# Performance work log

Measured on AMD Instinct MI355X. Metric: run time of the kernel, lower is better.

## Reference

```python
import jax, jax.numpy as jnp
import numpy as np

DIM = 768
NUM_HEADS = 12
HIDDEN = int(DIM * 4.0)
EPS = 1e-5


def setup_inputs() -> dict:
    key = jax.random.key(0)
    ks = jax.random.split(key, 8)
    s = lambda k, shape, scale=0.02: jax.random.normal(k, shape, dtype=jnp.float32) * scale
    return {
        "x": jax.random.normal(ks[0], (8, 1024, DIM), dtype=jnp.float32),
        "ln1_g": jnp.ones((DIM,), jnp.float32),
        "ln1_b": jnp.zeros((DIM,), jnp.float32),
        "qkv_w": s(ks[1], (DIM, 3 * DIM)),
        "qkv_b": jnp.zeros((3 * DIM,), jnp.float32),
        "proj_w": s(ks[2], (DIM, DIM)),
        "proj_b": jnp.zeros((DIM,), jnp.float32),
        "ln2_g": jnp.ones((DIM,), jnp.float32),
        "ln2_b": jnp.zeros((DIM,), jnp.float32),
        "fc1_w": s(ks[3], (DIM, HIDDEN)),
        "fc1_b": jnp.zeros((HIDDEN,), jnp.float32),
        "fc2_w": s(ks[4], (HIDDEN, DIM)),
        "fc2_b": jnp.zeros((DIM,), jnp.float32),
    }


def layer_norm(x, g, b):
    mu = jnp.mean(x, axis=-1, keepdims=True)
    var = jnp.mean(jnp.square(x - mu), axis=-1, keepdims=True)
    return (x - mu) * jax.lax.rsqrt(var + EPS) * g + b


def reference(x, ln1_g, ln1_b, qkv_w, qkv_b, proj_w, proj_b,
              ln2_g, ln2_b, fc1_w, fc1_b, fc2_w, fc2_b):
    B, N, C = x.shape
    H = NUM_HEADS
    Dh = C // H
    scale = Dh ** -0.5

    # --- Attention (pre-norm) ---
    h = layer_norm(x, ln1_g, ln1_b)
    qkv = h @ qkv_w + qkv_b                       # [B, N, 3C]
    qkv = qkv.reshape(B, N, 3, H, Dh)
    q, k, v = qkv[:, :, 0], qkv[:, :, 1], qkv[:, :, 2]  # [B, N, H, Dh]
    attn = jnp.einsum("bqhd,bkhd->bhqk", q, k) * scale  # [B, H, N, N]
    attn = jax.nn.softmax(attn, axis=-1)
    o = jnp.einsum("bhqk,bkhd->bqhd", attn, v).reshape(B, N, C)
    x = x + (o @ proj_w + proj_b)

    # --- MLP (pre-norm) ---
    h = layer_norm(x, ln2_g, ln2_b)
    h = jax.nn.gelu(h @ fc1_w + fc1_b, approximate=False)  # torch nn.GELU = exact erf
    x = x + (h @ fc2_w + fc2_b)
    return x
```

## Files before the change

kernel.cpp:

```cpp
#include <hip/hip_runtime.h>
#include <hip/hip_bf16.h>
#include <cstdint>

using f32x4  = __attribute__((ext_vector_type(4))) float;
using bf16x8 = __attribute__((ext_vector_type(8))) short;

__device__ inline ushort f2bf(float f) {
    union { float f; uint u; } x; x.f = f;
    uint u = x.u;
    return (ushort)((u + 0x7FFFu + ((u >> 16) & 1u)) >> 16);
}

__device__ inline void unpack8(uint4 v, float* out) {
    uint ws[4] = {v.x, v.y, v.z, v.w};
#pragma unroll
    for (int i = 0; i < 4; ++i) {
        union { uint u; float f; } lo, hi;
        lo.u = ws[i] << 16;
        hi.u = ws[i] & 0xFFFF0000u;
        out[2 * i]     = lo.f;
        out[2 * i + 1] = hi.f;
    }
}

__device__ inline void gload16(const ushort* g, ushort* lds) {
    __builtin_amdgcn_global_load_lds(
        (const __attribute__((address_space(1))) unsigned int*)g,
        (__attribute__((address_space(3))) unsigned int*)lds, 16, 0, 0);
}

__global__ __launch_bounds__(256) void transpose_cast(const float* __restrict__ w,
                                                      ushort* __restrict__ wt,
                                                      int K, int N) {
    __shared__ float tile[32][33];
    const int bn = blockIdx.x * 32;
    const int bk = blockIdx.y * 32;
    const int tx = threadIdx.x & 31, ty = threadIdx.x >> 5;
#pragma unroll
    for (int i = 0; i < 32; i += 8)
        tile[ty + i][tx] = w[(size_t)(bk + ty + i) * N + bn + tx];
    __syncthreads();
#pragma unroll
    for (int i = 0; i < 32; i += 8)
        wt[(size_t)(bn + ty + i) * K + bk + tx] = f2bf(tile[tx][ty + i]);
}

__global__ __launch_bounds__(256) void ln_bf16(const float* __restrict__ x,
                                               const float* __restrict__ g,
                                               const float* __restrict__ b,
                                               ushort* __restrict__ out) {
    const int row = blockIdx.x;
    const float* xr = x + (size_t)row * 768;
    const int t = threadIdx.x;
    float v0 = xr[t], v1 = xr[t + 256], v2 = xr[t + 512];
    float s  = v0 + v1 + v2;
    float sq = v0 * v0 + v1 * v1 + v2 * v2;
#pragma unroll
    for (int off = 32; off > 0; off >>= 1) {
        s  += __shfl_down(s, off);
        sq += __shfl_down(sq, off);
    }
    __shared__ float sa[4], sb[4];
    const int wv = t >> 6, lane = t & 63;
    if (lane == 0) { sa[wv] = s; sb[wv] = sq; }
    __syncthreads();
    s  = sa[0] + sa[1] + sa[2] + sa[3];
    sq = sb[0] + sb[1] + sb[2] + sb[3];
    const float mu   = s * (1.0f / 768.0f);
    const float var  = sq * (1.0f / 768.0f) - mu * mu;
    const float rstd = rsqrtf(var + 1e-5f);
    ushort* orow = out + (size_t)row * 768;
    orow[t]       = f2bf((v0 - mu) * rstd * g[t]       + b[t]);
    orow[t + 256] = f2bf((v1 - mu) * rstd * g[t + 256] + b[t + 256]);
    orow[t + 512] = f2bf((v2 - mu) * rstd * g[t + 512] + b[t + 512]);
}

template <int EPI>
__global__ __launch_bounds__(256) void gemm_bt(const ushort* __restrict__ A,
                                               const ushort* __restrict__ Bt,
                                               const float* __restrict__ bias,
                                               const float* __restrict__ resid,
                                               void* __restrict__ out,
                                               int M, int N, int K) {
    __shared__ ushort As[128 * 32];
    __shared__ ushort Bs[128 * 32];
    const int t    = threadIdx.x;
    const int lane = t & 63;
    const int w    = t >> 6;
    const int wr   = w >> 1, wc = w & 1;
    const int bm   = blockIdx.y * 128, bn = blockIdx.x * 128;
    const int lr   = lane >> 4, lc = lane & 15;
    const int srow = lane >> 2;
    const int sk8  = (lane & 3) * 8;

    const f32x4 fzero = {0.f, 0.f, 0.f, 0.f};
    f32x4 acc[4][4];
#pragma unroll
    for (int ai = 0; ai < 4; ++ai)
#pragma unroll
        for (int bj = 0; bj < 4; ++bj) acc[ai][bj] = fzero;

    const ushort* Ag0 = A  + (size_t)(bm + w * 16 + srow) * K + sk8;
    const ushort* Ag1 = Ag0 + (size_t)64 * K;
    const ushort* Bg0 = Bt + (size_t)(bn + w * 16 + srow) * K + sk8;
    const ushort* Bg1 = Bg0 + (size_t)64 * K;
    ushort* lA0 = &As[(w * 16) * 32];
    ushort* lA1 = &As[(64 + w * 16) * 32];
    ushort* lB0 = &Bs[(w * 16) * 32];
    ushort* lB1 = &Bs[(64 + w * 16) * 32];

    for (int kb = 0; kb < K; kb += 32) {
        __syncthreads();
        gload16(Ag0 + kb, lA0);
        gload16(Ag1 + kb, lA1);
        gload16(Bg0 + kb, lB0);
        gload16(Bg1 + kb, lB1);
        __syncthreads();
        bf16x8 af[4], bf[4];
#pragma unroll
        for (int ai = 0; ai < 4; ++ai)
            af[ai] = *(const bf16x8*)&As[(wr * 64 + ai * 16 + lc) * 32 + lr * 8];
#pragma unroll
        for (int bj = 0; bj < 4; ++bj)
            bf[bj] = *(const bf16x8*)&Bs[(wc * 64 + bj * 16 + lc) * 32 + lr * 8];
#pragma unroll
        for (int ai = 0; ai < 4; ++ai)
#pragma unroll
            for (int bj = 0; bj < 4; ++bj)
                acc[ai][bj] = __builtin_amdgcn_mfma_f32_16x16x32_bf16(af[ai], bf[bj],
                                                                      acc[ai][bj], 0, 0, 0);
    }

#pragma unroll
    for (int ai = 0; ai < 4; ++ai) {
#pragma unroll
        for (int bj = 0; bj < 4; ++bj) {
            int col  = bn + wc * 64 + bj * 16 + lc;
            float bs = bias[col];
#pragma unroll
            for (int j = 0; j < 4; ++j) {
                int row   = bm + wr * 64 + ai * 16 + lr * 4 + j;
                float val = acc[ai][bj][j] + bs;
                if (EPI == 1) {
                    val += resid[(size_t)row * N + col];
                    ((float*)out)[(size_t)row * N + col] = val;
                } else if (EPI == 2) {
                    val = 0.5f * val * (1.0f + erff(val * 0.70710678118f));
                    ((ushort*)out)[(size_t)row * N + col] = f2bf(val);
                } else {
                    ((ushort*)out)[(size_t)row * N + col] = f2bf(val);
                }
            }
        }
    }
}

__global__ __launch_bounds__(256) void attn_mfma(const ushort* __restrict__ qkv,
                                                 ushort* __restrict__ outb) {
    __shared__ ushort Kls[64 * 72];
    __shared__ ushort Vtls[64 * 72];
    __shared__ ushort Pls[4][32 * 72];

    const int bid = blockIdx.x;
    const int b   = bid / 96;
    const int rem = bid % 96;
    const int h   = rem >> 3;
    const int qc  = rem & 7;
    const int t    = threadIdx.x;
    const int w    = t >> 6;
    const int lane = t & 63;
    const int lr   = lane >> 4, lc = lane & 15;
    const int q0   = qc * 128 + w * 32;
    const size_t bbase = (size_t)b * 1024;

    bf16x8 qa[2][2];
#pragma unroll
    for (int rt = 0; rt < 2; ++rt)
#pragma unroll
        for (int ds = 0; ds < 2; ++ds) {
            uint4 u = *(const uint4*)(qkv + (bbase + q0 + rt * 16 + lc) * 2304 +
                                      h * 64 + ds * 32 + lr * 8);
            float tmp[8];
            unpack8(u, tmp);
            bf16x8 v;
#pragma unroll
            for (int j = 0; j < 8; ++j) v[j] = (short)f2bf(tmp[j] * 0.125f);
            qa[rt][ds] = v;
        }

    const f32x4 fzero = {0.f, 0.f, 0.f, 0.f};
    f32x4 O[2][4];
    float m[2][4], l[2][4];
#pragma unroll
    for (int rt = 0; rt < 2; ++rt) {
#pragma unroll
        for (int dt = 0; dt < 4; ++dt) O[rt][dt] = fzero;
#pragma unroll
        for (int j = 0; j < 4; ++j) { m[rt][j] = -INFINITY; l[rt][j] = 0.0f; }
    }

    for (int kt = 0; kt < 16; ++kt) {
        const int k0 = kt * 64;
        __syncthreads();
#pragma unroll
        for (int i = 0; i < 2; ++i) {
            int idx = t + i * 256;
            int key = idx >> 3, seg = idx & 7;
            uint4 u = *(const uint4*)(qkv + (bbase + k0 + key) * 2304 + 768 +
                                      h * 64 + seg * 8);
            *(uint4*)&Kls[key * 72 + seg * 8] = u;
        }
        {
            int key = t & 63, dblk = t >> 6;
#pragma unroll
            for (int i = 0; i < 2; ++i) {
                int d0 = dblk * 8 + i * 32;
                uint4 u = *(const uint4*)(qkv + (bbase + k0 + key) * 2304 + 1536 +
                                          h * 64 + d0);
                const ushort* us = (const ushort*)&u;
#pragma unroll
                for (int j = 0; j < 8; ++j) Vtls[(d0 + j) * 72 + key] = us[j];
            }
        }
        __syncthreads();

        f32x4 s4[2][4];
#pragma unroll
        for (int rt = 0; rt < 2; ++rt)
#pragma unroll
            for (int kt4 = 0; kt4 < 4; ++kt4) {
                f32x4 acc = fzero;
#pragma unroll
                for (int ds = 0; ds < 2; ++ds) {
                    bf16x8 kb = *(const bf16x8*)&Kls[(kt4 * 16 + lc) * 72 + ds * 32 + lr * 8];
                    acc = __builtin_amdgcn_mfma_f32_16x16x32_bf16(qa[rt][ds], kb, acc, 0, 0, 0);
                }
                s4[rt][kt4] = acc;
            }

#pragma unroll
        for (int rt = 0; rt < 2; ++rt) {
#pragma unroll
            for (int j = 0; j < 4; ++j) {
                float v = fmaxf(fmaxf(s4[rt][0][j], s4[rt][1][j]),
                                fmaxf(s4[rt][2][j], s4[rt][3][j]));
#pragma unroll
                for (int off = 1; off < 16; off <<= 1) v = fmaxf(v, __shfl_xor(v, off));
                float mn = fmaxf(m[rt][j], v);
                float c  = __expf(m[rt][j] - mn);
                m[rt][j] = mn;
                float psum = 0.f;
#pragma unroll
                for (int kt4 = 0; kt4 < 4; ++kt4) {
                    float p = __expf(s4[rt][kt4][j] - mn);
                    s4[rt][kt4][j] = p;
                    psum += p;
                }
#pragma unroll
                for (int off = 1; off < 16; off <<= 1) psum += __shfl_xor(psum, off);
                l[rt][j] = l[rt][j] * c + psum;
#pragma unroll
                for (int dt = 0; dt < 4; ++dt) O[rt][dt][j] *= c;
                int prow = rt * 16 + lr * 4 + j;
#pragma unroll
                for (int kt4 = 0; kt4 < 4; ++kt4)
                    Pls[w][prow * 72 + kt4 * 16 + lc] = f2bf(s4[rt][kt4][j]);
            }
        }

        bf16x8 pa[2][2];
#pragma unroll
        for (int rt = 0; rt < 2; ++rt)
#pragma unroll
            for (int ks = 0; ks < 2; ++ks)
                pa[rt][ks] = *(const bf16x8*)&Pls[w][(rt * 16 + lc) * 72 + ks * 32 + lr * 8];
#pragma unroll
        for (int dt = 0; dt < 4; ++dt)
#pragma unroll
            for (int ks = 0; ks < 2; ++ks) {
                bf16x8 vb = *(const bf16x8*)&Vtls[(dt * 16 + lc) * 72 + ks * 32 + lr * 8];
#pragma unroll
                for (int rt = 0; rt < 2; ++rt)
                    O[rt][dt] = __builtin_amdgcn_mfma_f32_16x16x32_bf16(pa[rt][ks], vb,
                                                                        O[rt][dt], 0, 0, 0);
            }
    }

#pragma unroll
    for (int rt = 0; rt < 2; ++rt)
#pragma unroll
        for (int j = 0; j < 4; ++j) {
            float inv = 1.0f / l[rt][j];
            size_t row = bbase + q0 + rt * 16 + lr * 4 + j;
#pragma unroll
            for (int dt = 0; dt < 4; ++dt)
                outb[row * 768 + h * 64 + dt * 16 + lc] = f2bf(O[rt][dt][j] * inv);
        }
}

extern "C" void kernel_launch(void* const* d_in, const int* in_sizes, int n_in,
                              void* d_out, int out_size, void* d_ws, size_t ws_size,
                              hipStream_t stream) {
    const float* x      = (const float*)d_in[0];
    const float* ln1_g  = (const float*)d_in[1];
    const float* ln1_b  = (const float*)d_in[2];
    const float* qkv_w  = (const float*)d_in[3];
    const float* qkv_b  = (const float*)d_in[4];
    const float* proj_w = (const float*)d_in[5];
    const float* proj_b = (const float*)d_in[6];
    const float* ln2_g  = (const float*)d_in[7];
    const float* ln2_b  = (const float*)d_in[8];
    const float* fc1_w  = (const float*)d_in[9];
    const float* fc1_b  = (const float*)d_in[10];
    const float* fc2_w  = (const float*)d_in[11];
    const float* fc2_b  = (const float*)d_in[12];

    char* ws = (char*)d_ws;
    auto alloc = [&](size_t bytes) {
        char* p = ws;
        ws += (bytes + 255) & ~(size_t)255;
        return p;
    };
    ushort* qkv_wt  = (ushort*)alloc((size_t)768 * 2304 * 2);
    ushort* proj_wt = (ushort*)alloc((size_t)768 * 768 * 2);
    ushort* fc1_wt  = (ushort*)alloc((size_t)768 * 3072 * 2);
    ushort* fc2_wt  = (ushort*)alloc((size_t)3072 * 768 * 2);
    ushort* hb      = (ushort*)alloc((size_t)8192 * 768 * 2);
    ushort* qkvb    = (ushort*)alloc((size_t)8192 * 2304 * 2);
    ushort* ob      = (ushort*)alloc((size_t)8192 * 768 * 2);
    float*  x1      = (float*)alloc((size_t)8192 * 768 * 4);
    ushort* h2b     = (ushort*)alloc((size_t)8192 * 768 * 2);
    ushort* h3b     = (ushort*)alloc((size_t)8192 * 3072 * 2);

    transpose_cast<<<dim3(2304 / 32, 768 / 32), 256, 0, stream>>>(qkv_w, qkv_wt, 768, 2304);
    transpose_cast<<<dim3(768 / 32, 768 / 32), 256, 0, stream>>>(proj_w, proj_wt, 768, 768);
    transpose_cast<<<dim3(3072 / 32, 768 / 32), 256, 0, stream>>>(fc1_w, fc1_wt, 768, 3072);
    transpose_cast<<<dim3(768 / 32, 3072 / 32), 256, 0, stream>>>(fc2_w, fc2_wt, 3072, 768);

    ln_bf16<<<8192, 256, 0, stream>>>(x, ln1_g, ln1_b, hb);
    gemm_bt<0><<<dim3(2304 / 128, 8192 / 128), 256, 0, stream>>>(hb, qkv_wt, qkv_b, nullptr,
                                                                 qkvb, 8192, 2304, 768);
    attn_mfma<<<8 * 12 * 8, 256, 0, stream>>>(qkvb, ob);
    gemm_bt<1><<<dim3(768 / 128, 8192 / 128), 256, 0, stream>>>(ob, proj_wt, proj_b, x,
                                                                x1, 8192, 768, 768);
    ln_bf16<<<8192, 256, 0, stream>>>(x1, ln2_g, ln2_b, h2b);
    gemm_bt<2><<<dim3(3072 / 128, 8192 / 128), 256, 0, stream>>>(h2b, fc1_wt, fc1_b, nullptr,
                                                                 h3b, 8192, 3072, 768);
    gemm_bt<1><<<dim3(768 / 128, 8192 / 128), 256, 0, stream>>>(h3b, fc2_wt, fc2_b, x1,
                                                                (float*)d_out, 8192, 768, 3072);
}
```

Before: 347.6 us.

## Double GEMM K-tile to 64 and use lazy-rescale exp2 softmax in attention

The GEMM now stages a 128x64 K-slice per barrier pair instead of 128x32, halving the number of sync/load rounds and issuing two MFMA sub-steps per tile. The attention kernel folds log2(e) into the Q scale so it can use exp2f, and rescales the running max, sum and output only when the new max exceeds the old by more than 8, which skips most rescale multiplies. The lazy rescale lets probabilities grow up to 2^8 before renormalising, which stays safe in fp32 but increases bf16 P values. LDS use in the GEMM doubles.

Result: slower. 397.0 us (+14.2%).

```diff
diff --git a/kernel.cpp b/kernel.cpp
--- a/kernel.cpp
+++ b/kernel.cpp
@@ -82,16 +82,14 @@
                                                const float* __restrict__ resid,
                                                void* __restrict__ out,
                                                int M, int N, int K) {
-    __shared__ ushort As[128 * 32];
-    __shared__ ushort Bs[128 * 32];
+    __shared__ ushort As[128 * 64];
+    __shared__ ushort Bs[128 * 64];
+    const int bm   = blockIdx.y * 128, bn = blockIdx.x * 128;
     const int t    = threadIdx.x;
     const int lane = t & 63;
     const int w    = t >> 6;
     const int wr   = w >> 1, wc = w & 1;
-    const int bm   = blockIdx.y * 128, bn = blockIdx.x * 128;
     const int lr   = lane >> 4, lc = lane & 15;
-    const int srow = lane >> 2;
-    const int sk8  = (lane & 3) * 8;
 
     const f32x4 fzero = {0.f, 0.f, 0.f, 0.f};
     f32x4 acc[4][4];
@@ -100,35 +98,44 @@
 #pragma unroll
         for (int bj = 0; bj < 4; ++bj) acc[ai][bj] = fzero;
 
-    const ushort* Ag0 = A  + (size_t)(bm + w * 16 + srow) * K + sk8;
-    const ushort* Ag1 = Ag0 + (size_t)64 * K;
-    const ushort* Bg0 = Bt + (size_t)(bn + w * 16 + srow) * K + sk8;
-    const ushort* Bg1 = Bg0 + (size_t)64 * K;
-    ushort* lA0 = &As[(w * 16) * 32];
-    ushort* lA1 = &As[(64 + w * 16) * 32];
-    ushort* lB0 = &Bs[(w * 16) * 32];
-    ushort* lB1 = &Bs[(64 + w * 16) * 32];
-
-    for (int kb = 0; kb < K; kb += 32) {
+    const int srow = lane >> 3, sk8 = (lane & 7) * 8;
+    const ushort* Ag[4];
+    const ushort* Bg[4];
+    ushort* lA[4];
+    ushort* lB[4];
+#pragma unroll
+    for (int i = 0; i < 4; ++i) {
+        int j = w * 4 + i;
+        Ag[i] = A  + (size_t)(bm + j * 8 + srow) * K + sk8;
+        Bg[i] = Bt + (size_t)(bn + j * 8 + srow) * K + sk8;
+        lA[i] = &As[j * 512];
+        lB[i] = &Bs[j * 512];
+    }
+
+    for (int kb = 0; kb < K; kb += 64) {
         __syncthreads();
-        gload16(Ag0 + kb, lA0);
-        gload16(Ag1 + kb, lA1);
-        gload16(Bg0 + kb, lB0);
-        gload16(Bg1 + kb, lB1);
+#pragma unroll
+        for (int i = 0; i < 4; ++i) {
+            gload16(Ag[i] + kb, lA[i]);
+            gload16(Bg[i] + kb, lB[i]);
+        }
         __syncthreads();
-        bf16x8 af[4], bf[4];
-#pragma unroll
-        for (int ai = 0; ai < 4; ++ai)
-            af[ai] = *(const bf16x8*)&As[(wr * 64 + ai * 16 + lc) * 32 + lr * 8];
-#pragma unroll
-        for (int bj = 0; bj < 4; ++bj)
-            bf[bj] = *(const bf16x8*)&Bs[(wc * 64 + bj * 16 + lc) * 32 + lr * 8];
-#pragma unroll
-        for (int ai = 0; ai < 4; ++ai)
+#pragma unroll
+        for (int ks = 0; ks < 2; ++ks) {
+            bf16x8 af[4], bf[4];
+#pragma unroll
+            for (int ai = 0; ai < 4; ++ai)
+                af[ai] = *(const bf16x8*)&As[(wr * 64 + ai * 16 + lc) * 64 + ks * 32 + lr * 8];
 #pragma unroll
             for (int bj = 0; bj < 4; ++bj)
-                acc[ai][bj] = __builtin_amdgcn_mfma_f32_16x16x32_bf16(af[ai], bf[bj],
-                                                                      acc[ai][bj], 0, 0, 0);
+                bf[bj] = *(const bf16x8*)&Bs[(wc * 64 + bj * 16 + lc) * 64 + ks * 32 + lr * 8];
+#pragma unroll
+            for (int ai = 0; ai < 4; ++ai)
+#pragma unroll
+                for (int bj = 0; bj < 4; ++bj)
+                    acc[ai][bj] = __builtin_amdgcn_mfma_f32_16x16x32_bf16(af[ai], bf[bj],
+                                                                          acc[ai][bj], 0, 0, 0);
+        }
     }
 
 #pragma unroll
@@ -173,6 +180,7 @@
     const int q0   = qc * 128 + w * 32;
     const size_t bbase = (size_t)b * 1024;
 
+    const float qscale = 0.125f * 1.44269504088896f;
     bf16x8 qa[2][2];
 #pragma unroll
     for (int rt = 0; rt < 2; ++rt)
@@ -184,7 +192,7 @@
             unpack8(u, tmp);
             bf16x8 v;
 #pragma unroll
-            for (int j = 0; j < 8; ++j) v[j] = (short)f2bf(tmp[j] * 0.125f);
+            for (int j = 0; j < 8; ++j) v[j] = (short)f2bf(tmp[j] * qscale);
             qa[rt][ds] = v;
         }
 
@@ -246,25 +254,25 @@
                                 fmaxf(s4[rt][2][j], s4[rt][3][j]));
 #pragma unroll
                 for (int off = 1; off < 16; off <<= 1) v = fmaxf(v, __shfl_xor(v, off));
-                float mn = fmaxf(m[rt][j], v);
-                float c  = __expf(m[rt][j] - mn);
-                m[rt][j] = mn;
+                float mn = m[rt][j];
+                if (v > mn + 8.0f) {
+                    float c = exp2f(mn - v);
+                    mn = v; m[rt][j] = v;
+                    l[rt][j] *= c;
+#pragma unroll
+                    for (int dt = 0; dt < 4; ++dt) O[rt][dt][j] *= c;
+                }
                 float psum = 0.f;
+                int prow = rt * 16 + lr * 4 + j;
 #pragma unroll
                 for (int kt4 = 0; kt4 < 4; ++kt4) {
-                    float p = __expf(s4[rt][kt4][j] - mn);
-                    s4[rt][kt4][j] = p;
+                    float p = exp2f(s4[rt][kt4][j] - mn);
                     psum += p;
+                    Pls[w][prow * 72 + kt4 * 16 + lc] = f2bf(p);
                 }
 #pragma unroll
                 for (int off = 1; off < 16; off <<= 1) psum += __shfl_xor(psum, off);
-                l[rt][j] = l[rt][j] * c + psum;
-#pragma unroll
-                for (int dt = 0; dt < 4; ++dt) O[rt][dt][j] *= c;
-                int prow = rt * 16 + lr * 4 + j;
-#pragma unroll
-                for (int kt4 = 0; kt4 < 4; ++kt4)
-                    Pls[w][prow * 72 + kt4 * 16 + lc] = f2bf(s4[rt][kt4][j]);
+                l[rt][j] += psum;
             }
         }
 
@@ -340,7 +348,7 @@
     ln_bf16<<<8192, 256, 0, stream>>>(x, ln1_g, ln1_b, hb);
     gemm_bt<0><<<dim3(2304 / 128, 8192 / 128), 256, 0, stream>>>(hb, qkv_wt, qkv_b, nullptr,
                                                                  qkvb, 8192, 2304, 768);
-    attn_mfma<<<8 * 12 * 8, 256, 0, stream>>>(qkvb, ob);
+    attn_mfma<<<768, 256, 0, stream>>>(qkvb, ob);
     gemm_bt<1><<<dim3(768 / 128, 8192 / 128), 256, 0, stream>>>(ob, proj_wt, proj_b, x,
                                                                 x1, 8192, 768, 768);
     ln_bf16<<<8192, 256, 0, stream>>>(x1, ln2_g, ln2_b, h2b);
```
